# Performance work log

Measured on AMD Instinct MI355X. Metric: run time of the kernel, lower is better.

Reference implementation:

```python
import jax, jax.numpy as jnp
import numpy as np

N = 20000      # nodes
E = 400000     # directed edges
F_IN = 256     # node features
H, C = 16, 32  # heads, per-head channels (out_channels + beta_on, beta_on=0)
OUT = 32       # out_channels
HID = 128      # 4 * out_channels


def setup_inputs() -> dict:
    key = jax.random.key(0)
    ks = jax.random.split(key, 14)
    s = 0.05
    return {
        "x": jax.random.normal(ks[0], (N, F_IN), jnp.float32),
        "edge_index": jax.random.randint(ks[1], (2, E), 0, N, jnp.int32),
        "W1": jax.random.normal(ks[2], (F_IN, H * C), jnp.float32) * s,
        "att_src1": jax.random.normal(ks[3], (H, C), jnp.float32) * s,
        "att_dst1": jax.random.normal(ks[4], (H, C), jnp.float32) * s,
        "b1": jax.random.normal(ks[5], (C,), jnp.float32) * s,
        "W2": jax.random.normal(ks[6], (F_IN, H * C), jnp.float32) * s,
        "att_src2": jax.random.normal(ks[7], (H, C), jnp.float32) * s,
        "att_dst2": jax.random.normal(ks[8], (H, C), jnp.float32) * s,
        "b2": jax.random.normal(ks[9], (C,), jnp.float32) * s,
        "lin1_w": jax.random.normal(ks[10], (F_IN, HID), jnp.float32) * s,
        "lin1_b": jax.random.normal(ks[11], (HID,), jnp.float32) * s,
        "lin2_w": jax.random.normal(ks[12], (HID, OUT), jnp.float32) * s,
        "lin2_b": jax.random.normal(ks[13], (OUT,), jnp.float32) * s,
    }


def gat_conv(x, W, att_src, att_dst, bias, src, dst):
    """PyG GATConv: heads=H, concat=False (mean over heads), no self loops.
    src = message source node per edge, dst = aggregation (central) node."""
    h = (x @ W).reshape(-1, H, C)                 # [N, H, C]
    a_s = jnp.sum(h * att_src, axis=-1)           # [N, H]
    a_d = jnp.sum(h * att_dst, axis=-1)           # [N, H]
    alpha = jax.nn.leaky_relu(a_s[src] + a_d[dst], 0.2)  # [E, H]
    # numerically-stable segment softmax over edges grouped by dst
    m = jax.lax.stop_gradient(jax.ops.segment_max(alpha, dst, num_segments=N))
    m = jnp.where(jnp.isfinite(m), m, 0.0)        # empty segments -> -inf
    ex = jnp.exp(alpha - m[dst])                  # [E, H]
    den = jax.ops.segment_sum(ex, dst, num_segments=N)   # [N, H]
    coef = ex / (den[dst] + 1e-16)                # [E, H]
    msg = h[src] * coef[:, :, None]               # [E, H, C]
    out = jax.ops.segment_sum(msg, dst, num_segments=N)  # [N, H, C]
    return out.mean(axis=1) + bias                # concat=False -> head mean


def reference(x, edge_index, W1, att_src1, att_dst1, b1, W2, att_src2, att_dst2,
              b2, lin1_w, lin1_b, lin2_w, lin2_b):
    src = edge_index[0]
    dst = edge_index[1]
    # conv1: flow='source_to_target' -> aggregate at edge_index[1]
    x_in = jax.nn.elu(gat_conv(x, W1, att_src1, att_dst1, b1, src, dst))
    # conv2: flow='target_to_source' -> aggregate at edge_index[0]
    x_out = jax.nn.elu(gat_conv(x, W2, att_src2, att_dst2, b2, dst, src))
    x1 = jax.nn.elu(x @ lin1_w + lin1_b)
    x_self = jax.nn.elu(x1 @ lin2_w + lin2_b)
    return (x_in, x_out, x_self)
```

## Files before the change

### kernel.cpp

```cpp
#include <hip/hip_runtime.h>
#include <math.h>

#define NN 20000
#define EE 400000
#define FIN 256
#define HH 16
#define CC 32
#define HC 512
#define H8W 1024
#define HIDN 128
#define OUTC 32
#define WT 1024

typedef unsigned short u16;
typedef unsigned char u8;
typedef __attribute__((ext_vector_type(8))) short short8v;
typedef __attribute__((ext_vector_type(4))) float f32x4;
typedef __attribute__((ext_vector_type(2))) float f32x2;

__device__ inline u16 f2bf(float f) {
  unsigned u = __builtin_bit_cast(unsigned, f);
  unsigned r = (u + 0x7fffu + ((u >> 16) & 1u)) >> 16;
  return (u16)r;
}
__device__ inline float bf2f(u16 b) {
  unsigned u = ((unsigned)b) << 16;
  return __builtin_bit_cast(float, u);
}

__device__ __forceinline__ void gload16(const u16* g, u16* l) {
  __builtin_amdgcn_global_load_lds(
      (const __attribute__((address_space(1))) unsigned int*)g,
      (__attribute__((address_space(3))) unsigned int*)l, 16, 0, 0);
}

__device__ __forceinline__ void fp8x8_fma(uint2 hv, float w, float* acc) {
  f32x2 p;
  p = __builtin_amdgcn_cvt_pk_f32_fp8(hv.x, false);
  acc[0] = fmaf(w, p.x, acc[0]); acc[1] = fmaf(w, p.y, acc[1]);
  p = __builtin_amdgcn_cvt_pk_f32_fp8(hv.x, true);
  acc[2] = fmaf(w, p.x, acc[2]); acc[3] = fmaf(w, p.y, acc[3]);
  p = __builtin_amdgcn_cvt_pk_f32_fp8(hv.y, false);
  acc[4] = fmaf(w, p.x, acc[4]); acc[5] = fmaf(w, p.y, acc[5]);
  p = __builtin_amdgcn_cvt_pk_f32_fp8(hv.y, true);
  acc[6] = fmaf(w, p.x, acc[6]); acc[7] = fmaf(w, p.y, acc[7]);
}

__global__ void k_prep_hist(const float* __restrict__ x, u16* __restrict__ xb,
                            const float* __restrict__ W1, const float* __restrict__ W2,
                            u16* __restrict__ wtc,
                            const float* __restrict__ L1, u16* __restrict__ lt1,
                            const float* __restrict__ L2, u16* __restrict__ lt2,
                            const int* __restrict__ ei, int* __restrict__ cur) {
  int b = blockIdx.x, t = threadIdx.x;
  if (b < 2500) {
    int i = b * 256 + t;
    float4 v0 = ((const float4*)x)[i * 2];
    float4 v1 = ((const float4*)x)[i * 2 + 1];
    short8v o;
    o[0] = (short)f2bf(v0.x); o[1] = (short)f2bf(v0.y);
    o[2] = (short)f2bf(v0.z); o[3] = (short)f2bf(v0.w);
    o[4] = (short)f2bf(v1.x); o[5] = (short)f2bf(v1.y);
    o[6] = (short)f2bf(v1.z); o[7] = (short)f2bf(v1.w);
    *(short8v*)(xb + (size_t)i * 8) = o;
  } else if (b < 3524) {
    int i = (b - 2500) * 256 + t;
    int n = i >> 8, k = i & 255;
    wtc[i] = f2bf(n < 512 ? W1[k * HC + n] : W2[k * HC + (n - 512)]);
  } else if (b < 3652) {
    int i = (b - 3524) * 256 + t;
    int n = i >> 8, k = i & 255;
    lt1[i] = f2bf(L1[k * HIDN + n]);
  } else if (b < 3668) {
    int i = (b - 3652) * 256 + t;
    int n = i >> 7, k = i & 127;
    lt2[i] = f2bf(L2[k * OUTC + n]);
  } else {
    int e = (b - 3668) * 256 + t;
    if (e < EE) {
      atomicAdd(&cur[ei[EE + e]], 1);
      atomicAdd(&cur[NN + ei[e]], 1);
    }
  }
}

__device__ void scan_one(int* cur, int* off, int* part) {
  const int t = threadIdx.x;
  const int CHK = 20;
  int base = t * CHK;
  int loc[CHK];
  int s = 0;
#pragma unroll
  for (int i = 0; i < CHK; ++i) {
    int idx = base + i;
    int v = (idx < NN) ? cur[idx] : 0;
    loc[i] = s;
    s += v;
  }
  part[t] = s;
  __syncthreads();
  for (int d = 1; d < 1024; d <<= 1) {
    int v2 = (t >= d) ? part[t - d] : 0;
    __syncthreads();
    part[t] += v2;
    __syncthreads();
  }
  int cbase = part[t] - s;
#pragma unroll
  for (int i = 0; i < CHK; ++i) {
    int idx = base + i;
    if (idx < NN) {
      int o = cbase + loc[i];
      off[idx] = o;
      cur[idx] = o;
    }
  }
  if (t == 1023) off[NN] = part[1023];
}

__global__ __launch_bounds__(1024) void k_scan(int* cur, int* off1, int* off2) {
  __shared__ int part[1024];
  if (blockIdx.x == 0) scan_one(cur, off1, part);
  else                 scan_one(cur + NN, off2, part);
}

__global__ void k_scatter(const int* __restrict__ ei, int* cur,
                          int* __restrict__ adj1, int* __restrict__ adj2) {
  int e = blockIdx.x * 256 + threadIdx.x;
  if (e < EE) {
    int s1 = ei[e], d1 = ei[EE + e];
    int p1 = atomicAdd(&cur[d1], 1);
    adj1[p1] = s1;
    int p2 = atomicAdd(&cur[NN + s1], 1);
    adj2[p2] = d1;
  }
}

__global__ __launch_bounds__(256) void k_gemm_big(const u16* __restrict__ A,
                                                  const u16* __restrict__ Bt,
                                                  const float* __restrict__ as1,
                                                  const float* __restrict__ ad1,
                                                  const float* __restrict__ as2,
                                                  const float* __restrict__ ad2,
                                                  u8* __restrict__ h8,
                                                  float* __restrict__ a_sA,
                                                  float* __restrict__ a_dA) {
  __shared__ u16 As[128 * 64];
  __shared__ u16 Bs[128 * 64];
  const int hw = blockIdx.x;
  const int logical = (hw & 7) * 157 + (hw >> 3);
  const int bm = (logical >> 3) * 128, bn = logical & 7;
  const int t = threadIdx.x;
  const int lane = t & 63, wave = t >> 6;
  const int wr = (wave >> 1) * 64, wc = (wave & 1) * 64;
  const int l15 = lane & 15, l4 = lane >> 4;
  const int rloc = lane >> 3;
  const int kc_src = (lane & 7) ^ rloc;
  const int K = FIN;

  f32x4 acc[4][4] = {};
  for (int k0 = 0; k0 < K; k0 += 64) {
    __syncthreads();
#pragma unroll
    for (int q = 0; q < 4; ++q) {
      const int rblk = q * 4 + wave;
      const int r = rblk * 8 + rloc;
      gload16(A + (size_t)(bm + r) * K + k0 + kc_src * 8, As + rblk * 512);
      gload16(Bt + (size_t)(bn * 128 + r) * K + k0 + kc_src * 8, Bs + rblk * 512);
    }
    __syncthreads();
#pragma unroll
    for (int kh = 0; kh < 2; ++kh) {
      const int kc = kh * 4 + l4;
      short8v af[4], bfr[4];
#pragma unroll
      for (int i = 0; i < 4; ++i) {
        int row = wr + i * 16 + l15;
        af[i] = *(const short8v*)(As + row * 64 + (kc ^ (row & 7)) * 8);
      }
#pragma unroll
      for (int j = 0; j < 4; ++j) {
        int row = wc + j * 16 + l15;
        bfr[j] = *(const short8v*)(Bs + row * 64 + (kc ^ (row & 7)) * 8);
      }
#pragma unroll
      for (int i = 0; i < 4; ++i)
#pragma unroll
        for (int j = 0; j < 4; ++j)
          acc[i][j] = __builtin_amdgcn_mfma_f32_16x16x32_bf16(af[i], bfr[j], acc[i][j], 0, 0, 0);
    }
  }

  const int conv = bn >> 2;
#pragma unroll
  for (int i = 0; i < 4; ++i)
#pragma unroll
    for (int j = 0; j < 4; ++j)
#pragma unroll
      for (int r = 0; r < 4; ++r) {
        int row = bm + wr + i * 16 + l4 * 4 + r;
        if (row >= NN) continue;
        int colb = bn * 128 + wc + j * 16 + l15;
        float v = acc[i][j][r];
        unsigned e8 = __builtin_amdgcn_cvt_pk_fp8_f32(v, v, 0, false);
        h8[(size_t)row * H8W + colb] = (u8)e8;
      }

  float asv[4], adv[4];
#pragma unroll
  for (int j = 0; j < 4; ++j) {
    int lc = (bn & 3) * 128 + wc + j * 16 + l15;
    int hh = lc >> 5, c = lc & 31;
    asv[j] = (conv ? as2 : as1)[hh * CC + c];
    adv[j] = (conv ? ad2 : ad1)[hh * CC + c];
  }
  const int hA = (bn & 3) * 4 + (wc >> 5);
  float* aS = a_sA + (size_t)conv * NN * HH;
  float* aD = a_dA + (size_t)conv * NN * HH;
#pragma unroll
  for (int i = 0; i < 4; ++i)
#pragma unroll
    for (int r = 0; r < 4; ++r) {
      float sAs = acc[i][0][r] * asv[0] + acc[i][1][r] * asv[1];
      float sAd = acc[i][0][r] * adv[0] + acc[i][1][r] * adv[1];
      float sBs = acc[i][2][r] * asv[2] + acc[i][3][r] * asv[3];
      float sBd = acc[i][2][r] * adv[2] + acc[i][3][r] * adv[3];
#pragma unroll
      for (int m = 1; m < 16; m <<= 1) {
        sAs += __shfl_xor(sAs, m);
        sAd += __shfl_xor(sAd, m);
        sBs += __shfl_xor(sBs, m);
        sBd += __shfl_xor(sBd, m);
      }
      int row = bm + wr + i * 16 + l4 * 4 + r;
      if (l15 == 0 && row < NN) {
        *(float2*)(aS + (size_t)row * HH + hA) = make_float2(sAs, sBs);
        *(float2*)(aD + (size_t)row * HH + hA) = make_float2(sAd, sBd);
      }
    }
}

__global__ __launch_bounds__(256) void k_self(const u16* __restrict__ A,
                                              const u16* __restrict__ lt1,
                                              const u16* __restrict__ lt2,
                                              const float* __restrict__ lin1_b,
                                              const float* __restrict__ lin2_b,
                                              float* __restrict__ outp) {
  __shared__ u16 smem[128 * 136];
  u16* As = smem;
  u16* Bs = smem + 128 * 64;
  const int t = threadIdx.x;
  const int lane = t & 63, wave = t >> 6;
  const int wr = (wave >> 1) * 64, wc = (wave & 1) * 64;
  const int bm = blockIdx.x * 128;
  const int l15 = lane & 15, l4 = lane >> 4;
  const int rloc = lane >> 3;
  const int kc_src = (lane & 7) ^ rloc;
  const int K = FIN;

  f32x4 acc[4][4] = {};
  for (int k0 = 0; k0 < K; k0 += 64) {
    __syncthreads();
#pragma unroll
    for (int q = 0; q < 4; ++q) {
      const int rblk = q * 4 + wave;
      const int r = rblk * 8 + rloc;
      gload16(A + (size_t)(bm + r) * K + k0 + kc_src * 8, As + rblk * 512);
      gload16(lt1 + (size_t)r * K + k0 + kc_src * 8, Bs + rblk * 512);
    }
    __syncthreads();
#pragma unroll
    for (int kh = 0; kh < 2; ++kh) {
      const int kc = kh * 4 + l4;
      short8v af[4], bfr[4];
#pragma unroll
      for (int i = 0; i < 4; ++i) {
        int row = wr + i * 16 + l15;
        af[i] = *(const short8v*)(As + row * 64 + (kc ^ (row & 7)) * 8);
      }
#pragma unroll
      for (int j = 0; j < 4; ++j) {
        int row = wc + j * 16 + l15;
        bfr[j] = *(const short8v*)(Bs + row * 64 + (kc ^ (row & 7)) * 8);
      }
#pragma unroll
      for (int i = 0; i < 4; ++i)
#pragma unroll
        for (int j = 0; j < 4; ++j)
          acc[i][j] = __builtin_amdgcn_mfma_f32_16x16x32_bf16(af[i], bfr[j], acc[i][j], 0, 0, 0);
    }
  }
  __syncthreads();
#pragma unroll
  for (int i = 0; i < 4; ++i)
#pragma unroll
    for (int j = 0; j < 4; ++j)
#pragma unroll
      for (int r = 0; r < 4; ++r) {
        int row = wr + i * 16 + l4 * 4 + r;
        int col = wc + j * 16 + l15;
        float v = acc[i][j][r] + lin1_b[col];
        v = v > 0.f ? v : (expf(v) - 1.f);
        smem[row * 136 + col] = f2bf(v);
      }
  __syncthreads();
  f32x4 acc2[2][2] = {};
#pragma unroll
  for (int kk = 0; kk < 4; ++kk) {
    short8v af[2], bfr[2];
#pragma unroll
    for (int i = 0; i < 2; ++i)
      af[i] = *(const short8v*)(smem + (wave * 32 + i * 16 + l15) * 136 + kk * 32 + l4 * 8);
#pragma unroll
    for (int j = 0; j < 2; ++j)
      bfr[j] = *(const short8v*)(lt2 + (size_t)(j * 16 + l15) * 128 + kk * 32 + l4 * 8);
#pragma unroll
    for (int i = 0; i < 2; ++i)
#pragma unroll
      for (int j = 0; j < 2; ++j)
        acc2[i][j] = __builtin_amdgcn_mfma_f32_16x16x32_bf16(af[i], bfr[j], acc2[i][j], 0, 0, 0);
  }
#pragma unroll
  for (int i = 0; i < 2; ++i)
#pragma unroll
    for (int j = 0; j < 2; ++j)
#pragma unroll
      for (int r = 0; r < 4; ++r) {
        int row = bm + wave * 32 + i * 16 + l4 * 4 + r;
        int col = j * 16 + l15;
        if (row < NN) {
          float v = acc2[i][j][r] + lin2_b[col];
          v = v > 0.f ? v : (expf(v) - 1.f);
          outp[(size_t)row * OUTC + col] = v;
        }
      }
}

__global__ __launch_bounds__(256) void k_edge(const int* __restrict__ adj1,
                                              const int* __restrict__ off1,
                                              const int* __restrict__ adj2,
                                              const int* __restrict__ off2,
                                              const float* __restrict__ a_sA,
                                              const float* __restrict__ a_dA,
                                              const u8* __restrict__ h8,
                                              const float* __restrict__ b1,
                                              const float* __restrict__ b2,
                                              float* __restrict__ out) {
  const int wv = threadIdx.x >> 6, lane = threadIdx.x & 63;
  const int gid = blockIdx.x * 4 + wv;
  const int conv = gid >= NN;
  const int node = gid - conv * NN;
  const int* __restrict__ adj = conv ? adj2 : adj1;
  const int* __restrict__ off = conv ? off2 : off1;
  const float* __restrict__ a_s = a_sA + (size_t)conv * NN * HH;
  const float* __restrict__ a_d = a_dA + (size_t)conv * NN * HH;
  const u8* __restrict__ hbase = h8 + conv * HC;
  const float* __restrict__ bias = conv ? b2 : b1;
  float* __restrict__ outp = out + (size_t)conv * NN * OUTC;
  const int e0 = off[node], e1 = off[node + 1];

  const int h = lane >> 2, coff = (lane & 3) * 8;
  const float adh = a_d[node * HH + h];
  float acc0[8] = {}, acc1[8] = {};
  float den = 0.f;
  int p = e0;
  for (; p + 4 <= e1; p += 4) {
    int s0 = adj[p], s1 = adj[p + 1], s2 = adj[p + 2], s3 = adj[p + 3];
    float al0 = a_s[s0 * HH + h] + adh;
    float al1 = a_s[s1 * HH + h] + adh;
    float al2 = a_s[s2 * HH + h] + adh;
    float al3 = a_s[s3 * HH + h] + adh;
    al0 = al0 > 0.f ? al0 : 0.2f * al0;
    al1 = al1 > 0.f ? al1 : 0.2f * al1;
    al2 = al2 > 0.f ? al2 : 0.2f * al2;
    al3 = al3 > 0.f ? al3 : 0.2f * al3;
    float w0 = __expf(al0), w1 = __expf(al1), w2 = __expf(al2), w3 = __expf(al3);
    uint2 h0 = *(const uint2*)(hbase + (size_t)s0 * H8W + h * CC + coff);
    uint2 h1 = *(const uint2*)(hbase + (size_t)s1 * H8W + h * CC + coff);
    uint2 h2 = *(const uint2*)(hbase + (size_t)s2 * H8W + h * CC + coff);
    uint2 h3 = *(const uint2*)(hbase + (size_t)s3 * H8W + h * CC + coff);
    den += (w0 + w1) + (w2 + w3);
    fp8x8_fma(h0, w0, acc0);
    fp8x8_fma(h1, w1, acc1);
    fp8x8_fma(h2, w2, acc0);
    fp8x8_fma(h3, w3, acc1);
  }
  for (; p < e1; ++p) {
    int s0 = adj[p];
    float al0 = a_s[s0 * HH + h] + adh;
    al0 = al0 > 0.f ? al0 : 0.2f * al0;
    float w0 = __expf(al0);
    uint2 h0 = *(const uint2*)(hbase + (size_t)s0 * H8W + h * CC + coff);
    den += w0;
    fp8x8_fma(h0, w0, acc0);
  }
  const float ivh = (1.f / 16.f) / (den + 1e-16f);
  float accf[8];
#pragma unroll
  for (int i = 0; i < 8; ++i) accf[i] = (acc0[i] + acc1[i]) * ivh;
#pragma unroll
  for (int mk = 4; mk <= 32; mk <<= 1)
#pragma unroll
    for (int i = 0; i < 8; ++i) accf[i] += __shfl_xor(accf[i], mk);
  if (lane < 4) {
#pragma unroll
    for (int i = 0; i < 8; ++i) {
      int c = coff + i;
      float v = accf[i] + bias[c];
      v = v > 0.f ? v : (expf(v) - 1.f);
      outp[(size_t)node * OUTC + c] = v;
    }
  }
}

extern "C" void kernel_launch(void* const* d_in, const int* in_sizes, int n_in,
                              void* d_out, int out_size, void* d_ws, size_t ws_size,
                              hipStream_t stream) {
  const float* x = (const float*)d_in[0];
  const int* ei = (const int*)d_in[1];
  const float* W1 = (const float*)d_in[2];
  const float* att_src1 = (const float*)d_in[3];
  const float* att_dst1 = (const float*)d_in[4];
  const float* b1 = (const float*)d_in[5];
  const float* W2 = (const float*)d_in[6];
  const float* att_src2 = (const float*)d_in[7];
  const float* att_dst2 = (const float*)d_in[8];
  const float* b2 = (const float*)d_in[9];
  const float* lin1_w = (const float*)d_in[10];
  const float* lin1_b = (const float*)d_in[11];
  const float* lin2_w = (const float*)d_in[12];
  const float* lin2_b = (const float*)d_in[13];
  float* out = (float*)d_out;

  char* w = (char*)d_ws;
  u8* h8 = (u8*)w;          w += (size_t)NN * H8W;
  u16* x_bf = (u16*)w;      w += (size_t)NN * FIN * 2;
  u16* wtc = (u16*)w;       w += (size_t)WT * FIN * 2;
  u16* lt1 = (u16*)w;       w += (size_t)HIDN * FIN * 2;
  u16* lt2 = (u16*)w;       w += (size_t)OUTC * HIDN * 2;
  float* a_sA = (float*)w;  w += (size_t)2 * NN * HH * 4;
  float* a_dA = (float*)w;  w += (size_t)2 * NN * HH * 4;
  int* off1 = (int*)w;      w += (size_t)(NN + 1) * 4;
  int* off2 = (int*)w;      w += (size_t)(NN + 1) * 4;
  int* cur = (int*)w;       w += (size_t)2 * NN * 4;
  int* adj1 = (int*)w;      w += (size_t)EE * 4;
  int* adj2 = (int*)w;      w += (size_t)EE * 4;

  const int EB = (EE + 255) / 256;

  hipMemsetAsync(cur, 0, (size_t)2 * NN * 4, stream);
  k_prep_hist<<<3668 + EB, 256, 0, stream>>>(x, x_bf, W1, W2, wtc, lin1_w, lt1,
                                             lin2_w, lt2, ei, cur);
  k_scan<<<2, 1024, 0, stream>>>(cur, off1, off2);
  k_scatter<<<EB, 256, 0, stream>>>(ei, cur, adj1, adj2);

  k_gemm_big<<<1256, 256, 0, stream>>>(x_bf, wtc, att_src1, att_dst1,
                                       att_src2, att_dst2, h8, a_sA, a_dA);
  k_self<<<157, 256, 0, stream>>>(x_bf, lt1, lt2, lin1_b, lin2_b,
                                  out + (size_t)2 * NN * OUTC);

  k_edge<<<2 * (NN / 4), 256, 0, stream>>>(adj1, off1, adj2, off2, a_sA, a_dA,
                                           h8, b1, b2, out);
}
```

Measured before the change: 232.5 us.

## Fuse scatter, GAT GEMM and self-MLP into one launch; widen edge-kernel loads

Merges the edge scatter, the big projection GEMM and the self MLP kernels into a single launch whose blocks branch on index range. Independent work can then overlap and two launches disappear. The self-MLP hidden tile in LDS moves to an XOR-swizzled 128-wide layout. Separately, the edge aggregation kernel now has each lane load 16 fp8 channels (uint4) and has the two half-waves process different edges, combining them with a cross-half shuffle. This means fewer, wider gathers but more registers per lane.

```diff
diff --git a/kernel.cpp b/kernel.cpp
--- a/kernel.cpp
+++ b/kernel.cpp
@@ -12,6 +12,10 @@
 #define OUTC 32
 #define WT 1024
 
+#define SCAT_B 1563
+#define GEMM_B 1256
+#define SELF_B 157
+
 typedef unsigned short u16;
 typedef unsigned char u8;
 typedef __attribute__((ext_vector_type(8))) short short8v;
@@ -34,16 +38,24 @@
       (__attribute__((address_space(3))) unsigned int*)l, 16, 0, 0);
 }
 
-__device__ __forceinline__ void fp8x8_fma(uint2 hv, float w, float* acc) {
+__device__ __forceinline__ void fp8x16_fma(uint4 hv, float w, float* acc) {
   f32x2 p;
   p = __builtin_amdgcn_cvt_pk_f32_fp8(hv.x, false);
-  acc[0] = fmaf(w, p.x, acc[0]); acc[1] = fmaf(w, p.y, acc[1]);
+  acc[0] = fmaf(w, p.x, acc[0]);  acc[1] = fmaf(w, p.y, acc[1]);
   p = __builtin_amdgcn_cvt_pk_f32_fp8(hv.x, true);
-  acc[2] = fmaf(w, p.x, acc[2]); acc[3] = fmaf(w, p.y, acc[3]);
+  acc[2] = fmaf(w, p.x, acc[2]);  acc[3] = fmaf(w, p.y, acc[3]);
   p = __builtin_amdgcn_cvt_pk_f32_fp8(hv.y, false);
-  acc[4] = fmaf(w, p.x, acc[4]); acc[5] = fmaf(w, p.y, acc[5]);
+  acc[4] = fmaf(w, p.x, acc[4]);  acc[5] = fmaf(w, p.y, acc[5]);
   p = __builtin_amdgcn_cvt_pk_f32_fp8(hv.y, true);
-  acc[6] = fmaf(w, p.x, acc[6]); acc[7] = fmaf(w, p.y, acc[7]);
+  acc[6] = fmaf(w, p.x, acc[6]);  acc[7] = fmaf(w, p.y, acc[7]);
+  p = __builtin_amdgcn_cvt_pk_f32_fp8(hv.z, false);
+  acc[8] = fmaf(w, p.x, acc[8]);  acc[9] = fmaf(w, p.y, acc[9]);
+  p = __builtin_amdgcn_cvt_pk_f32_fp8(hv.z, true);
+  acc[10] = fmaf(w, p.x, acc[10]); acc[11] = fmaf(w, p.y, acc[11]);
+  p = __builtin_amdgcn_cvt_pk_f32_fp8(hv.w, false);
+  acc[12] = fmaf(w, p.x, acc[12]); acc[13] = fmaf(w, p.y, acc[13]);
+  p = __builtin_amdgcn_cvt_pk_f32_fp8(hv.w, true);
+  acc[14] = fmaf(w, p.x, acc[14]); acc[15] = fmaf(w, p.y, acc[15]);
 }
 
 __global__ void k_prep_hist(const float* __restrict__ x, u16* __restrict__ xb,
@@ -124,216 +136,215 @@
   else                 scan_one(cur + NN, off2, part);
 }
 
-__global__ void k_scatter(const int* __restrict__ ei, int* cur,
-                          int* __restrict__ adj1, int* __restrict__ adj2) {
-  int e = blockIdx.x * 256 + threadIdx.x;
-  if (e < EE) {
-    int s1 = ei[e], d1 = ei[EE + e];
-    int p1 = atomicAdd(&cur[d1], 1);
-    adj1[p1] = s1;
-    int p2 = atomicAdd(&cur[NN + s1], 1);
-    adj2[p2] = d1;
-  }
-}
-
-__global__ __launch_bounds__(256) void k_gemm_big(const u16* __restrict__ A,
-                                                  const u16* __restrict__ Bt,
-                                                  const float* __restrict__ as1,
-                                                  const float* __restrict__ ad1,
-                                                  const float* __restrict__ as2,
-                                                  const float* __restrict__ ad2,
-                                                  u8* __restrict__ h8,
-                                                  float* __restrict__ a_sA,
-                                                  float* __restrict__ a_dA) {
-  __shared__ u16 As[128 * 64];
-  __shared__ u16 Bs[128 * 64];
-  const int hw = blockIdx.x;
-  const int logical = (hw & 7) * 157 + (hw >> 3);
-  const int bm = (logical >> 3) * 128, bn = logical & 7;
+__global__ __launch_bounds__(256) void k_main(const int* __restrict__ ei, int* cur,
+                                              int* __restrict__ adj1, int* __restrict__ adj2,
+                                              const u16* __restrict__ A,
+                                              const u16* __restrict__ Bt,
+                                              const float* __restrict__ as1,
+                                              const float* __restrict__ ad1,
+                                              const float* __restrict__ as2,
+                                              const float* __restrict__ ad2,
+                                              u8* __restrict__ h8,
+                                              float* __restrict__ a_sA,
+                                              float* __restrict__ a_dA,
+                                              const u16* __restrict__ lt1,
+                                              const u16* __restrict__ lt2,
+                                              const float* __restrict__ lin1_b,
+                                              const float* __restrict__ lin2_b,
+                                              float* __restrict__ out3) {
+  __shared__ u16 smem[128 * 128];
+  u16* As = smem;
+  u16* Bs = smem + 128 * 64;
+  const int b = blockIdx.x;
   const int t = threadIdx.x;
+
+  if (b < SCAT_B) {
+    int e = b * 256 + t;
+    if (e < EE) {
+      int s1 = ei[e], d1 = ei[EE + e];
+      int p1 = atomicAdd(&cur[d1], 1);
+      adj1[p1] = s1;
+      int p2 = atomicAdd(&cur[NN + s1], 1);
+      adj2[p2] = d1;
+    }
+    return;
+  }
+
   const int lane = t & 63, wave = t >> 6;
-  const int wr = (wave >> 1) * 64, wc = (wave & 1) * 64;
   const int l15 = lane & 15, l4 = lane >> 4;
   const int rloc = lane >> 3;
   const int kc_src = (lane & 7) ^ rloc;
   const int K = FIN;
 
-  f32x4 acc[4][4] = {};
-  for (int k0 = 0; k0 < K; k0 += 64) {
+  if (b < SCAT_B + GEMM_B) {
+    const int hw = b - SCAT_B;
+    const int logical = (hw & 7) * 157 + (hw >> 3);
+    const int bm = (logical >> 3) * 128, bn = logical & 7;
+    const int wr = (wave >> 1) * 64, wc = (wave & 1) * 64;
+
+    f32x4 acc[4][4] = {};
+    for (int k0 = 0; k0 < K; k0 += 64) {
+      __syncthreads();
+#pragma unroll
+      for (int q = 0; q < 4; ++q) {
+        const int rblk = q * 4 + wave;
+        const int r = rblk * 8 + rloc;
+        gload16(A + (size_t)(bm + r) * K + k0 + kc_src * 8, As + rblk * 512);
+        gload16(Bt + (size_t)(bn * 128 + r) * K + k0 + kc_src * 8, Bs + rblk * 512);
+      }
+      __syncthreads();
+#pragma unroll
+      for (int kh = 0; kh < 2; ++kh) {
+        const int kc = kh * 4 + l4;
+        short8v af[4], bfr[4];
+#pragma unroll
+        for (int i = 0; i < 4; ++i) {
+          int row = wr + i * 16 + l15;
+          af[i] = *(const short8v*)(As + row * 64 + (kc ^ (row & 7)) * 8);
+        }
+#pragma unroll
+        for (int j = 0; j < 4; ++j) {
+          int row = wc + j * 16 + l15;
+          bfr[j] = *(const short8v*)(Bs + row * 64 + (kc ^ (row & 7)) * 8);
+        }
+#pragma unroll
+        for (int i = 0; i < 4; ++i)
+#pragma unroll
+          for (int j = 0; j < 4; ++j)
+            acc[i][j] = __builtin_amdgcn_mfma_f32_16x16x32_bf16(af[i], bfr[j], acc[i][j], 0, 0, 0);
+      }
+    }
+
+    const int conv = bn >> 2;
+#pragma unroll
+    for (int i = 0; i < 4; ++i)
+#pragma unroll
+      for (int j = 0; j < 4; ++j)
+#pragma unroll
+        for (int r = 0; r < 4; ++r) {
+          int row = bm + wr + i * 16 + l4 * 4 + r;
+          if (row >= NN) continue;
+          int colb = bn * 128 + wc + j * 16 + l15;
+          float v = acc[i][j][r];
+          unsigned e8 = __builtin_amdgcn_cvt_pk_fp8_f32(v, v, 0, false);
+          h8[(size_t)row * H8W + colb] = (u8)e8;
+        }
+
+    float asv[4], adv[4];
+#pragma unroll
+    for (int j = 0; j < 4; ++j) {
+      int lc = (bn & 3) * 128 + wc + j * 16 + l15;
+      int hh = lc >> 5, c = lc & 31;
+      asv[j] = (conv ? as2 : as1)[hh * CC + c];
+      adv[j] = (conv ? ad2 : ad1)[hh * CC + c];
+    }
+    const int hA = (bn & 3) * 4 + (wc >> 5);
+    float* aS = a_sA + (size_t)conv * NN * HH;
+    float* aD = a_dA + (size_t)conv * NN * HH;
+#pragma unroll
+    for (int i = 0; i < 4; ++i)
+#pragma unroll
+      for (int r = 0; r < 4; ++r) {
+        float sAs = acc[i][0][r] * asv[0] + acc[i][1][r] * asv[1];
+        float sAd = acc[i][0][r] * adv[0] + acc[i][1][r] * adv[1];
+        float sBs = acc[i][2][r] * asv[2] + acc[i][3][r] * asv[3];
+        float sBd = acc[i][2][r] * adv[2] + acc[i][3][r] * adv[3];
+#pragma unroll
+        for (int m = 1; m < 16; m <<= 1) {
+          sAs += __shfl_xor(sAs, m);
+          sAd += __shfl_xor(sAd, m);
+          sBs += __shfl_xor(sBs, m);
+          sBd += __shfl_xor(sBd, m);
+        }
+        int row = bm + wr + i * 16 + l4 * 4 + r;
+        if (l15 == 0 && row < NN) {
+          *(float2*)(aS + (size_t)row * HH + hA) = make_float2(sAs, sBs);
+          *(float2*)(aD + (size_t)row * HH + hA) = make_float2(sAd, sBd);
+        }
+      }
+  } else {
+    const int bm = (b - SCAT_B - GEMM_B) * 128;
+    const int wr = (wave >> 1) * 64, wc = (wave & 1) * 64;
+
+    f32x4 acc[4][4] = {};
+    for (int k0 = 0; k0 < K; k0 += 64) {
+      __syncthreads();
+#pragma unroll
+      for (int q = 0; q < 4; ++q) {
+        const int rblk = q * 4 + wave;
+        const int r = rblk * 8 + rloc;
+        gload16(A + (size_t)(bm + r) * K + k0 + kc_src * 8, As + rblk * 512);
+        gload16(lt1 + (size_t)r * K + k0 + kc_src * 8, Bs + rblk * 512);
+      }
+      __syncthreads();
+#pragma unroll
+      for (int kh = 0; kh < 2; ++kh) {
+        const int kc = kh * 4 + l4;
+        short8v af[4], bfr[4];
+#pragma unroll
+        for (int i = 0; i < 4; ++i) {
+          int row = wr + i * 16 + l15;
+          af[i] = *(const short8v*)(As + row * 64 + (kc ^ (row & 7)) * 8);
+        }
+#pragma unroll
+        for (int j = 0; j < 4; ++j) {
+          int row = wc + j * 16 + l15;
+          bfr[j] = *(const short8v*)(Bs + row * 64 + (kc ^ (row & 7)) * 8);
+        }
+#pragma unroll
+        for (int i = 0; i < 4; ++i)
+#pragma unroll
+          for (int j = 0; j < 4; ++j)
+            acc[i][j] = __builtin_amdgcn_mfma_f32_16x16x32_bf16(af[i], bfr[j], acc[i][j], 0, 0, 0);
+      }
+    }
     __syncthreads();
 #pragma unroll
-    for (int q = 0; q < 4; ++q) {
-      const int rblk = q * 4 + wave;
-      const int r = rblk * 8 + rloc;
-      gload16(A + (size_t)(bm + r) * K + k0 + kc_src * 8, As + rblk * 512);
-      gload16(Bt + (size_t)(bn * 128 + r) * K + k0 + kc_src * 8, Bs + rblk * 512);
-    }
+    for (int i = 0; i < 4; ++i)
+#pragma unroll
+      for (int j = 0; j < 4; ++j)
+#pragma unroll
+        for (int r = 0; r < 4; ++r) {
+          int row = wr + i * 16 + l4 * 4 + r;
+          int col = wc + j * 16 + l15;
+          float v = acc[i][j][r] + lin1_b[col];
+          v = v > 0.f ? v : (expf(v) - 1.f);
+          smem[row * 128 + ((((col >> 3) ^ (row & 7))) << 3) + (col & 7)] = f2bf(v);
+        }
     __syncthreads();
-#pragma unroll
-    for (int kh = 0; kh < 2; ++kh) {
-      const int kc = kh * 4 + l4;
-      short8v af[4], bfr[4];
-#pragma unroll
-      for (int i = 0; i < 4; ++i) {
-        int row = wr + i * 16 + l15;
-        af[i] = *(const short8v*)(As + row * 64 + (kc ^ (row & 7)) * 8);
-      }
-#pragma unroll
-      for (int j = 0; j < 4; ++j) {
-        int row = wc + j * 16 + l15;
-        bfr[j] = *(const short8v*)(Bs + row * 64 + (kc ^ (row & 7)) * 8);
-      }
-#pragma unroll
-      for (int i = 0; i < 4; ++i)
-#pragma unroll
-        for (int j = 0; j < 4; ++j)
-          acc[i][j] = __builtin_amdgcn_mfma_f32_16x16x32_bf16(af[i], bfr[j], acc[i][j], 0, 0, 0);
-    }
-  }
-
-  const int conv = bn >> 2;
-#pragma unroll
-  for (int i = 0; i < 4; ++i)
-#pragma unroll
-    for (int j = 0; j < 4; ++j)
-#pragma unroll
-      for (int r = 0; r < 4; ++r) {
-        int row = bm + wr + i * 16 + l4 * 4 + r;
-        if (row >= NN) continue;
-        int colb = bn * 128 + wc + j * 16 + l15;
-        float v = acc[i][j][r];
-        unsigned e8 = __builtin_amdgcn_cvt_pk_fp8_f32(v, v, 0, false);
-        h8[(size_t)row * H8W + colb] = (u8)e8;
-      }
-
-  float asv[4], adv[4];
-#pragma unroll
-  for (int j = 0; j < 4; ++j) {
-    int lc = (bn & 3) * 128 + wc + j * 16 + l15;
-    int hh = lc >> 5, c = lc & 31;
-    asv[j] = (conv ? as2 : as1)[hh * CC + c];
-    adv[j] = (conv ? ad2 : ad1)[hh * CC + c];
-  }
-  const int hA = (bn & 3) * 4 + (wc >> 5);
-  float* aS = a_sA + (size_t)conv * NN * HH;
-  float* aD = a_dA + (size_t)conv * NN * HH;
-#pragma unroll
-  for (int i = 0; i < 4; ++i)
-#pragma unroll
-    for (int r = 0; r < 4; ++r) {
-      float sAs = acc[i][0][r] * asv[0] + acc[i][1][r] * asv[1];
-      float sAd = acc[i][0][r] * adv[0] + acc[i][1][r] * adv[1];
-      float sBs = acc[i][2][r] * asv[2] + acc[i][3][r] * asv[3];
-      float sBd = acc[i][2][r] * adv[2] + acc[i][3][r] * adv[3];
-#pragma unroll
-      for (int m = 1; m < 16; m <<= 1) {
-        sAs += __shfl_xor(sAs, m);
-        sAd += __shfl_xor(sAd, m);
-        sBs += __shfl_xor(sBs, m);
-        sBd += __shfl_xor(sBd, m);
-      }
-      int row = bm + wr + i * 16 + l4 * 4 + r;
-      if (l15 == 0 && row < NN) {
-        *(float2*)(aS + (size_t)row * HH + hA) = make_float2(sAs, sBs);
-        *(float2*)(aD + (size_t)row * HH + hA) = make_float2(sAd, sBd);
-      }
-    }
-}
-
-__global__ __launch_bounds__(256) void k_self(const u16* __restrict__ A,
-                                              const u16* __restrict__ lt1,
-                                              const u16* __restrict__ lt2,
-                                              const float* __restrict__ lin1_b,
-                                              const float* __restrict__ lin2_b,
-                                              float* __restrict__ outp) {
-  __shared__ u16 smem[128 * 136];
-  u16* As = smem;
-  u16* Bs = smem + 128 * 64;
-  const int t = threadIdx.x;
-  const int lane = t & 63, wave = t >> 6;
-  const int wr = (wave >> 1) * 64, wc = (wave & 1) * 64;
-  const int bm = blockIdx.x * 128;
-  const int l15 = lane & 15, l4 = lane >> 4;
-  const int rloc = lane >> 3;
-  const int kc_src = (lane & 7) ^ rloc;
-  const int K = FIN;
-
-  f32x4 acc[4][4] = {};
-  for (int k0 = 0; k0 < K; k0 += 64) {
-    __syncthreads();
-#pragma unroll
-    for (int q = 0; q < 4; ++q) {
-      const int rblk = q * 4 + wave;
-      const int r = rblk * 8 + rloc;
-      gload16(A + (size_t)(bm + r) * K + k0 + kc_src * 8, As + rblk * 512);
-      gload16(lt1 + (size_t)r * K + k0 + kc_src * 8, Bs + rblk * 512);
-    }
-    __syncthreads();
-#pragma unroll
-    for (int kh = 0; kh < 2; ++kh) {
-      const int kc = kh * 4 + l4;
-      short8v af[4], bfr[4];
-#pragma unroll
-      for (int i = 0; i < 4; ++i) {
-        int row = wr + i * 16 + l15;
-        af[i] = *(const short8v*)(As + row * 64 + (kc ^ (row & 7)) * 8);
-      }
-#pragma unroll
-      for (int j = 0; j < 4; ++j) {
-        int row = wc + j * 16 + l15;
-        bfr[j] = *(const short8v*)(Bs + row * 64 + (kc ^ (row & 7)) * 8);
-      }
-#pragma unroll
-      for (int i = 0; i < 4; ++i)
-#pragma unroll
-        for (int j = 0; j < 4; ++j)
-          acc[i][j] = __builtin_amdgcn_mfma_f32_16x16x32_bf16(af[i], bfr[j], acc[i][j], 0, 0, 0);
-    }
-  }
-  __syncthreads();
-#pragma unroll
-  for (int i = 0; i < 4; ++i)
-#pragma unroll
-    for (int j = 0; j < 4; ++j)
-#pragma unroll
-      for (int r = 0; r < 4; ++r) {
-        int row = wr + i * 16 + l4 * 4 + r;
-        int col = wc + j * 16 + l15;
-        float v = acc[i][j][r] + lin1_b[col];
-        v = v > 0.f ? v : (expf(v) - 1.f);
-        smem[row * 136 + col] = f2bf(v);
-      }
-  __syncthreads();
-  f32x4 acc2[2][2] = {};
-#pragma unroll
-  for (int kk = 0; kk < 4; ++kk) {
-    short8v af[2], bfr[2];
+    f32x4 acc2[2][2] = {};
+#pragma unroll
+    for (int kk = 0; kk < 4; ++kk) {
+      short8v af[2], bfr[2];
+#pragma unroll
+      for (int i = 0; i < 2; ++i) {
+        int row2 = wave * 32 + i * 16 + l15;
+        af[i] = *(const short8v*)(smem + row2 * 128 + (((kk * 4 + l4) ^ (row2 & 7)) << 3));
+      }
+#pragma unroll
+      for (int j = 0; j < 2; ++j)
+        bfr[j] = *(const short8v*)(lt2 + (size_t)(j * 16 + l15) * 128 + kk * 32 + l4 * 8);
+#pragma unroll
+      for (int i = 0; i < 2; ++i)
+#pragma unroll
+        for (int j = 0; j < 2; ++j)
+          acc2[i][j] = __builtin_amdgcn_mfma_f32_16x16x32_bf16(af[i], bfr[j], acc2[i][j], 0, 0, 0);
+    }
 #pragma unroll
     for (int i = 0; i < 2; ++i)
-      af[i] = *(const short8v*)(smem + (wave * 32 + i * 16 + l15) * 136 + kk * 32 + l4 * 8);
-#pragma unroll
-    for (int j = 0; j < 2; ++j)
-      bfr[j] = *(const short8v*)(lt2 + (size_t)(j * 16 + l15) * 128 + kk * 32 + l4 * 8);
-#pragma unroll
-    for (int i = 0; i < 2; ++i)
 #pragma unroll
       for (int j = 0; j < 2; ++j)
-        acc2[i][j] = __builtin_amdgcn_mfma_f32_16x16x32_bf16(af[i], bfr[j], acc2[i][j], 0, 0, 0);
-  }
-#pragma unroll
-  for (int i = 0; i < 2; ++i)
-#pragma unroll
-    for (int j = 0; j < 2; ++j)
-#pragma unroll
-      for (int r = 0; r < 4; ++r) {
-        int row = bm + wave * 32 + i * 16 + l4 * 4 + r;
-        int col = j * 16 + l15;
-        if (row < NN) {
-          float v = acc2[i][j][r] + lin2_b[col];
-          v = v > 0.f ? v : (expf(v) - 1.f);
-          outp[(size_t)row * OUTC + col] = v;
-        }
-      }
+#pragma unroll
+        for (int r = 0; r < 4; ++r) {
+          int row = bm + wave * 32 + i * 16 + l4 * 4 + r;
+          int col = j * 16 + l15;
+          if (row < NN) {
+            float v = acc2[i][j][r] + lin2_b[col];
+            v = v > 0.f ? v : (expf(v) - 1.f);
+            out3[(size_t)row * OUTC + col] = v;
+          }
+        }
+  }
 }
 
 __global__ __launch_bounds__(256) void k_edge(const int* __restrict__ adj1,
@@ -354,58 +365,69 @@
   const int* __restrict__ off = conv ? off2 : off1;
   const float* __restrict__ a_s = a_sA + (size_t)conv * NN * HH;
   const float* __restrict__ a_d = a_dA + (size_t)conv * NN * HH;
-  const u8* __restrict__ hbase = h8 + conv * HC;
   const float* __restrict__ bias = conv ? b2 : b1;
   float* __restrict__ outp = out + (size_t)conv * NN * OUTC;
   const int e0 = off[node], e1 = off[node + 1];
 
-  const int h = lane >> 2, coff = (lane & 3) * 8;
+  const int eh = lane >> 5, l5 = lane & 31;
+  const int h = l5 >> 1, half = l5 & 1;
+  const u8* hb = h8 + conv * HC + h * CC + half * 16;
   const float adh = a_d[node * HH + h];
-  float acc0[8] = {}, acc1[8] = {};
+  float acc0[16] = {}, acc1[16] = {};
   float den = 0.f;
   int p = e0;
   for (; p + 4 <= e1; p += 4) {
-    int s0 = adj[p], s1 = adj[p + 1], s2 = adj[p + 2], s3 = adj[p + 3];
-    float al0 = a_s[s0 * HH + h] + adh;
-    float al1 = a_s[s1 * HH + h] + adh;
-    float al2 = a_s[s2 * HH + h] + adh;
-    float al3 = a_s[s3 * HH + h] + adh;
-    al0 = al0 > 0.f ? al0 : 0.2f * al0;
-    al1 = al1 > 0.f ? al1 : 0.2f * al1;
-    al2 = al2 > 0.f ? al2 : 0.2f * al2;
-    al3 = al3 > 0.f ? al3 : 0.2f * al3;
-    float w0 = __expf(al0), w1 = __expf(al1), w2 = __expf(al2), w3 = __expf(al3);
-    uint2 h0 = *(const uint2*)(hbase + (size_t)s0 * H8W + h * CC + coff);
-    uint2 h1 = *(const uint2*)(hbase + (size_t)s1 * H8W + h * CC + coff);
-    uint2 h2 = *(const uint2*)(hbase + (size_t)s2 * H8W + h * CC + coff);
-    uint2 h3 = *(const uint2*)(hbase + (size_t)s3 * H8W + h * CC + coff);
-    den += (w0 + w1) + (w2 + w3);
-    fp8x8_fma(h0, w0, acc0);
-    fp8x8_fma(h1, w1, acc1);
-    fp8x8_fma(h2, w2, acc0);
-    fp8x8_fma(h3, w3, acc1);
-  }
-  for (; p < e1; ++p) {
-    int s0 = adj[p];
-    float al0 = a_s[s0 * HH + h] + adh;
-    al0 = al0 > 0.f ? al0 : 0.2f * al0;
-    float w0 = __expf(al0);
-    uint2 h0 = *(const uint2*)(hbase + (size_t)s0 * H8W + h * CC + coff);
-    den += w0;
-    fp8x8_fma(h0, w0, acc0);
-  }
+    int sA = adj[p + eh], sB = adj[p + 2 + eh];
+    float alA = a_s[sA * HH + h] + adh;
+    float alB = a_s[sB * HH + h] + adh;
+    alA = alA > 0.f ? alA : 0.2f * alA;
+    alB = alB > 0.f ? alB : 0.2f * alB;
+    float wA = __expf(alA), wB = __expf(alB);
+    uint4 hA = *(const uint4*)(hb + (size_t)sA * H8W);
+    uint4 hB = *(const uint4*)(hb + (size_t)sB * H8W);
+    den += wA + wB;
+    fp8x16_fma(hA, wA, acc0);
+    fp8x16_fma(hB, wB, acc1);
+  }
+  {
+    int pp = p + eh;
+    if (pp < e1) {
+      int s = adj[pp];
+      float al = a_s[s * HH + h] + adh;
+      al = al > 0.f ? al : 0.2f * al;
+      float wA = __expf(al);
+      uint4 hA = *(const uint4*)(hb + (size_t)s * H8W);
+      den += wA;
+      fp8x16_fma(hA, wA, acc0);
+    }
+    pp = p + 2 + eh;
+    if (pp < e1) {
+      int s = adj[pp];
+      float al = a_s[s * HH + h] + adh;
+      al = al > 0.f ? al : 0.2f * al;
+      float wB = __expf(al);
+      uint4 hB = *(const uint4*)(hb + (size_t)s * H8W);
+      den += wB;
+      fp8x16_fma(hB, wB, acc1);
+    }
+  }
+  float accf[16];
+#pragma unroll
+  for (int i = 0; i < 16; ++i) accf[i] = acc0[i] + acc1[i];
+  den += __shfl_xor(den, 32);
+#pragma unroll
+  for (int i = 0; i < 16; ++i) accf[i] += __shfl_xor(accf[i], 32);
   const float ivh = (1.f / 16.f) / (den + 1e-16f);
-  float accf[8];
-#pragma unroll
-  for (int i = 0; i < 8; ++i) accf[i] = (acc0[i] + acc1[i]) * ivh;
-#pragma unroll
-  for (int mk = 4; mk <= 32; mk <<= 1)
-#pragma unroll
-    for (int i = 0; i < 8; ++i) accf[i] += __shfl_xor(accf[i], mk);
-  if (lane < 4) {
-#pragma unroll
-    for (int i = 0; i < 8; ++i) {
-      int c = coff + i;
+#pragma unroll
+  for (int i = 0; i < 16; ++i) accf[i] *= ivh;
+#pragma unroll
+  for (int mk = 2; mk <= 16; mk <<= 1)
+#pragma unroll
+    for (int i = 0; i < 16; ++i) accf[i] += __shfl_xor(accf[i], mk);
+  if (lane < 2) {
+#pragma unroll
+    for (int i = 0; i < 16; ++i) {
+      int c = half * 16 + i;
       float v = accf[i] + bias[c];
       v = v > 0.f ? v : (expf(v) - 1.f);
       outp[(size_t)node * OUTC + c] = v;
@@ -452,12 +474,10 @@
   k_prep_hist<<<3668 + EB, 256, 0, stream>>>(x, x_bf, W1, W2, wtc, lin1_w, lt1,
                                              lin2_w, lt2, ei, cur);
   k_scan<<<2, 1024, 0, stream>>>(cur, off1, off2);
-  k_scatter<<<EB, 256, 0, stream>>>(ei, cur, adj1, adj2);
-
-  k_gemm_big<<<1256, 256, 0, stream>>>(x_bf, wtc, att_src1, att_dst1,
-                                       att_src2, att_dst2, h8, a_sA, a_dA);
-  k_self<<<157, 256, 0, stream>>>(x_bf, lt1, lt2, lin1_b, lin2_b,
-                                  out + (size_t)2 * NN * OUTC);
+
+  k_main<<<SCAT_B + GEMM_B + SELF_B, 256, 0, stream>>>(
+      ei, cur, adj1, adj2, x_bf, wtc, att_src1, att_dst1, att_src2, att_dst2,
+      h8, a_sA, a_dA, lt1, lt2, lin1_b, lin2_b, out + (size_t)2 * NN * OUTC);
 
   k_edge<<<2 * (NN / 4), 256, 0, stream>>>(adj1, off1, adj2, off2, a_sA, a_dA,
                                            h8, b1, b2, out);
```

Measured after the change: 237.1 us. 1.02x slower.

## Deduplicate edge attention compute across lanes, use packed FMA, swizzle LDS

Applied to the files above, without the earlier changes.

In the edge aggregation kernel, attention logits are now computed once per (edge, head) pair. Each of the 64 lanes handles one edge of a group of four for one head, and the resulting weights are broadcast with shuffles. This replaces the old scheme where four lanes recomputed the same exp and a_s load. The softmax denominator is reduced across lane groups at the end. The fp8 accumulate now uses packed float2 multiply-add, and the k_self second-stage LDS buffer switches from padding to an XOR swizzle, which saves shared memory. The cost is extra shuffles and a more complex tail path.

```diff
diff --git a/kernel.cpp b/kernel.cpp
--- a/kernel.cpp
+++ b/kernel.cpp
@@ -34,16 +34,16 @@
       (__attribute__((address_space(3))) unsigned int*)l, 16, 0, 0);
 }
 
-__device__ __forceinline__ void fp8x8_fma(uint2 hv, float w, float* acc) {
-  f32x2 p;
-  p = __builtin_amdgcn_cvt_pk_f32_fp8(hv.x, false);
-  acc[0] = fmaf(w, p.x, acc[0]); acc[1] = fmaf(w, p.y, acc[1]);
-  p = __builtin_amdgcn_cvt_pk_f32_fp8(hv.x, true);
-  acc[2] = fmaf(w, p.x, acc[2]); acc[3] = fmaf(w, p.y, acc[3]);
-  p = __builtin_amdgcn_cvt_pk_f32_fp8(hv.y, false);
-  acc[4] = fmaf(w, p.x, acc[4]); acc[5] = fmaf(w, p.y, acc[5]);
-  p = __builtin_amdgcn_cvt_pk_f32_fp8(hv.y, true);
-  acc[6] = fmaf(w, p.x, acc[6]); acc[7] = fmaf(w, p.y, acc[7]);
+__device__ __forceinline__ void fp8x8_fma2(uint2 hv, float w, f32x2* acc) {
+  f32x2 w2; w2.x = w; w2.y = w;
+  f32x2 p0 = __builtin_amdgcn_cvt_pk_f32_fp8(hv.x, false);
+  f32x2 p1 = __builtin_amdgcn_cvt_pk_f32_fp8(hv.x, true);
+  f32x2 p2 = __builtin_amdgcn_cvt_pk_f32_fp8(hv.y, false);
+  f32x2 p3 = __builtin_amdgcn_cvt_pk_f32_fp8(hv.y, true);
+  acc[0] += p0 * w2;
+  acc[1] += p1 * w2;
+  acc[2] += p2 * w2;
+  acc[3] += p3 * w2;
 }
 
 __global__ void k_prep_hist(const float* __restrict__ x, u16* __restrict__ xb,
@@ -246,7 +246,7 @@
                                               const float* __restrict__ lin1_b,
                                               const float* __restrict__ lin2_b,
                                               float* __restrict__ outp) {
-  __shared__ u16 smem[128 * 136];
+  __shared__ u16 smem[128 * 128];
   u16* As = smem;
   u16* Bs = smem + 128 * 64;
   const int t = threadIdx.x;
@@ -301,7 +301,7 @@
         int col = wc + j * 16 + l15;
         float v = acc[i][j][r] + lin1_b[col];
         v = v > 0.f ? v : (expf(v) - 1.f);
-        smem[row * 136 + col] = f2bf(v);
+        smem[row * 128 + ((((col >> 3) ^ (row & 7))) << 3) + (col & 7)] = f2bf(v);
       }
   __syncthreads();
   f32x4 acc2[2][2] = {};
@@ -309,8 +309,10 @@
   for (int kk = 0; kk < 4; ++kk) {
     short8v af[2], bfr[2];
 #pragma unroll
-    for (int i = 0; i < 2; ++i)
-      af[i] = *(const short8v*)(smem + (wave * 32 + i * 16 + l15) * 136 + kk * 32 + l4 * 8);
+    for (int i = 0; i < 2; ++i) {
+      int row2 = wave * 32 + i * 16 + l15;
+      af[i] = *(const short8v*)(smem + row2 * 128 + (((kk * 4 + l4) ^ (row2 & 7)) << 3));
+    }
 #pragma unroll
     for (int j = 0; j < 2; ++j)
       bfr[j] = *(const short8v*)(lt2 + (size_t)(j * 16 + l15) * 128 + kk * 32 + l4 * 8);
@@ -354,50 +356,77 @@
   const int* __restrict__ off = conv ? off2 : off1;
   const float* __restrict__ a_s = a_sA + (size_t)conv * NN * HH;
   const float* __restrict__ a_d = a_dA + (size_t)conv * NN * HH;
-  const u8* __restrict__ hbase = h8 + conv * HC;
   const float* __restrict__ bias = conv ? b2 : b1;
   float* __restrict__ outp = out + (size_t)conv * NN * OUTC;
   const int e0 = off[node], e1 = off[node + 1];
 
-  const int h = lane >> 2, coff = (lane & 3) * 8;
-  const float adh = a_d[node * HH + h];
-  float acc0[8] = {}, acc1[8] = {};
+  const int ea = lane >> 4, hh = lane & 15;
+  const int h = lane >> 2, cg = lane & 3;
+  const u8* hb = h8 + conv * HC + h * CC + cg * 8;
+  const float adh = a_d[node * HH + hh];
+  f32x2 acc0[4] = {}, acc1[4] = {};
   float den = 0.f;
   int p = e0;
   for (; p + 4 <= e1; p += 4) {
+    int se = adj[p + ea];
+    float al = a_s[se * HH + hh] + adh;
+    al = al > 0.f ? al : 0.2f * al;
+    float wgt = __expf(al);
+    den += wgt;
+    float w0 = __shfl(wgt, h);
+    float w1 = __shfl(wgt, 16 + h);
+    float w2 = __shfl(wgt, 32 + h);
+    float w3 = __shfl(wgt, 48 + h);
     int s0 = adj[p], s1 = adj[p + 1], s2 = adj[p + 2], s3 = adj[p + 3];
-    float al0 = a_s[s0 * HH + h] + adh;
-    float al1 = a_s[s1 * HH + h] + adh;
-    float al2 = a_s[s2 * HH + h] + adh;
-    float al3 = a_s[s3 * HH + h] + adh;
-    al0 = al0 > 0.f ? al0 : 0.2f * al0;
-    al1 = al1 > 0.f ? al1 : 0.2f * al1;
-    al2 = al2 > 0.f ? al2 : 0.2f * al2;
-    al3 = al3 > 0.f ? al3 : 0.2f * al3;
-    float w0 = __expf(al0), w1 = __expf(al1), w2 = __expf(al2), w3 = __expf(al3);
-    uint2 h0 = *(const uint2*)(hbase + (size_t)s0 * H8W + h * CC + coff);
-    uint2 h1 = *(const uint2*)(hbase + (size_t)s1 * H8W + h * CC + coff);
-    uint2 h2 = *(const uint2*)(hbase + (size_t)s2 * H8W + h * CC + coff);
-    uint2 h3 = *(const uint2*)(hbase + (size_t)s3 * H8W + h * CC + coff);
-    den += (w0 + w1) + (w2 + w3);
-    fp8x8_fma(h0, w0, acc0);
-    fp8x8_fma(h1, w1, acc1);
-    fp8x8_fma(h2, w2, acc0);
-    fp8x8_fma(h3, w3, acc1);
-  }
-  for (; p < e1; ++p) {
-    int s0 = adj[p];
-    float al0 = a_s[s0 * HH + h] + adh;
-    al0 = al0 > 0.f ? al0 : 0.2f * al0;
-    float w0 = __expf(al0);
-    uint2 h0 = *(const uint2*)(hbase + (size_t)s0 * H8W + h * CC + coff);
-    den += w0;
-    fp8x8_fma(h0, w0, acc0);
-  }
-  const float ivh = (1.f / 16.f) / (den + 1e-16f);
+    uint2 h0 = *(const uint2*)(hb + (size_t)s0 * H8W);
+    uint2 h1 = *(const uint2*)(hb + (size_t)s1 * H8W);
+    uint2 h2v = *(const uint2*)(hb + (size_t)s2 * H8W);
+    uint2 h3 = *(const uint2*)(hb + (size_t)s3 * H8W);
+    fp8x8_fma2(h0, w0, acc0);
+    fp8x8_fma2(h1, w1, acc1);
+    fp8x8_fma2(h2v, w2, acc0);
+    fp8x8_fma2(h3, w3, acc1);
+  }
+  if (p < e1) {
+    int pe = p + ea;
+    float wgt = 0.f;
+    if (pe < e1) {
+      int se = adj[pe];
+      float al = a_s[se * HH + hh] + adh;
+      al = al > 0.f ? al : 0.2f * al;
+      wgt = __expf(al);
+    }
+    den += wgt;
+    float w0 = __shfl(wgt, h);
+    float w1 = __shfl(wgt, 16 + h);
+    float w2 = __shfl(wgt, 32 + h);
+    {
+      int s0 = adj[p];
+      uint2 h0 = *(const uint2*)(hb + (size_t)s0 * H8W);
+      fp8x8_fma2(h0, w0, acc0);
+    }
+    if (p + 1 < e1) {
+      int s1 = adj[p + 1];
+      uint2 h1 = *(const uint2*)(hb + (size_t)s1 * H8W);
+      fp8x8_fma2(h1, w1, acc1);
+    }
+    if (p + 2 < e1) {
+      int s2 = adj[p + 2];
+      uint2 h2v = *(const uint2*)(hb + (size_t)s2 * H8W);
+      fp8x8_fma2(h2v, w2, acc0);
+    }
+  }
+  den += __shfl_xor(den, 16);
+  den += __shfl_xor(den, 32);
+  float inv = (1.f / 16.f) / (den + 1e-16f);
+  const float ivh = __shfl(inv, h);
   float accf[8];
 #pragma unroll
-  for (int i = 0; i < 8; ++i) accf[i] = (acc0[i] + acc1[i]) * ivh;
+  for (int i = 0; i < 4; ++i) {
+    f32x2 s2v = acc0[i] + acc1[i];
+    accf[2 * i] = s2v.x * ivh;
+    accf[2 * i + 1] = s2v.y * ivh;
+  }
 #pragma unroll
   for (int mk = 4; mk <= 32; mk <<= 1)
 #pragma unroll
@@ -405,7 +434,7 @@
   if (lane < 4) {
 #pragma unroll
     for (int i = 0; i < 8; ++i) {
-      int c = coff + i;
+      int c = cg * 8 + i;
       float v = accf[i] + bias[c];
       v = v > 0.f ? v : (expf(v) - 1.f);
       outp[(size_t)node * OUTC + c] = v;
```

Measured after the change: 238.9 us. 1.03x slower.
